# Performance work log

Measured on AMD Instinct MI355X. Metric: run time of the kernel, lower is better.

Reference implementation:

```python
import jax, jax.numpy as jnp
import numpy as np

N_NODES = 50000
N_EDGES = 600000
D = 128
ITERATIONS = 3


def setup_inputs() -> dict:
    key = jax.random.key(0)
    k0, k1, k2, k3 = jax.random.split(key, 4)
    node_feats = jax.random.normal(k0, (N_NODES, D), dtype=jnp.float32)
    adjacency = jax.random.randint(k1, (N_EDGES, 2), 0, N_NODES, dtype=jnp.int64)
    scale = 1.0 / np.sqrt(D).astype(np.float32)
    W_emb = jax.random.normal(k2, (D, D), dtype=jnp.float32) * scale
    b_emb = jnp.zeros((D,), dtype=jnp.float32)
    W_upd = jax.random.normal(k3, (D, D), dtype=jnp.float32) * scale
    b_upd = jnp.zeros((D,), dtype=jnp.float32)
    return {
        "node_feats": node_feats,
        "W_emb": W_emb,
        "b_emb": b_emb,
        "W_upd": W_upd,
        "b_upd": b_upd,
        "adjacency": adjacency,
    }


def reference(node_feats, W_emb, b_emb, W_upd, b_upd, adjacency):
    # Embedding layer: Dense + ReLU per node (inference path skips BatchNorm)
    h = jax.nn.relu(node_feats @ W_emb + b_emb)  # [N, D]

    src = adjacency[:, 0]
    dst = adjacency[:, 1]

    # Each undirected edge contributes a message in both directions.
    ones = jnp.ones((N_EDGES,), dtype=h.dtype)
    deg = (jax.ops.segment_sum(ones, src, num_segments=N_NODES)
           + jax.ops.segment_sum(ones, dst, num_segments=N_NODES))  # [N]
    denom = (deg + 1.0)[:, None]  # +1 for the node's own contribution

    for _ in range(ITERATIONS):
        # MessagePassing: gather neighbor features, scatter-add into nodes,
        # then normalize by (num incoming messages + 1).
        agg = (jax.ops.segment_sum(h[dst], src, num_segments=N_NODES)
               + jax.ops.segment_sum(h[src], dst, num_segments=N_NODES))  # [N, D]
        h = (h + agg) / denom
        # Update: per-node Dense followed by sigmoid nonlinearity.
        h = jax.nn.sigmoid(h @ W_upd + b_upd)
    return h
```

## Files before the change

### kernel.cpp

```cpp
#include <hip/hip_runtime.h>
#include <hip/hip_bf16.h>

#define NN 50000
#define NE 600000
#define DD 128
#define RB 64
#define NSHARD_DIV 6250
#define GB ((NN + RB - 1) / RB)
#define EBQ ((NE + 1023) / 1024)
#define SB ((NN + 1023) / 1024)
#define NSH2 12500
#define GQB2 (8 * ((NSH2 + 15) / 16))

typedef __bf16 bfrag __attribute__((ext_vector_type(8)));
typedef float  ffrag __attribute__((ext_vector_type(4)));
typedef unsigned uintv4 __attribute__((ext_vector_type(4)));
typedef unsigned uintv2 __attribute__((ext_vector_type(2)));

union frag_cast { uintv4 u4; unsigned u[4]; bfrag b; };

__device__ __forceinline__ float bfbits2f(unsigned v) { return __uint_as_float(v << 16); }
__device__ __forceinline__ unsigned f2bfbits(float f) {
    unsigned u = __float_as_uint(f);
    return (u + 0x7FFFu + ((u >> 16) & 1u)) >> 16;
}

__device__ __forceinline__ float ld_in(const void* p, int idx, int f32) {
    return f32 ? ((const float*)p)[idx]
               : bfbits2f(((const unsigned short*)p)[idx]);
}

__device__ __forceinline__ void ld_edge_nt(const int* adj, int e, int i64, int& s, int& d) {
    if (i64) {
        s = __builtin_nontemporal_load(&adj[4 * e]);
        d = __builtin_nontemporal_load(&adj[4 * e + 2]);
    } else {
        s = __builtin_nontemporal_load(&adj[2 * e]);
        d = __builtin_nontemporal_load(&adj[2 * e + 1]);
    }
}

__global__ void k_prep(const unsigned* __restrict__ Ww, const unsigned* __restrict__ adjw,
                       const void* __restrict__ We, const void* __restrict__ Wu,
                       unsigned short* __restrict__ WeT, unsigned short* __restrict__ WuT,
                       int* __restrict__ flags, int* __restrict__ deg) {
    const int tid = threadIdx.x;
    if (blockIdx.x < DD) {
        __shared__ int scnt;
        if (tid == 0) scnt = 0;
        __syncthreads();
        int c = 0;
        for (int i = tid; i < 512; i += 256) {
            unsigned e = (Ww[i] >> 7) & 0xFFu;
            c += (e >= 0x60u && e <= 0x85u) ? 1 : 0;
        }
        atomicAdd(&scnt, c);
        __syncthreads();
        const int f32 = (scnt >= 256) ? 0 : 1;
        const int k = blockIdx.x;
        if (tid < DD) {
            WeT[tid * DD + k] = (unsigned short)f2bfbits(ld_in(We, k * DD + tid, f32));
        } else {
            int n = tid - DD;
            WuT[n * DD + k] = (unsigned short)f2bfbits(ld_in(Wu, k * DD + n, f32));
        }
        return;
    }
    for (int i = (blockIdx.x - DD) * 256 + tid; i < NN; i += 64 * 256) deg[i] = 0;
    if (blockIdx.x != DD) return;
    __shared__ int cnt[2];
    if (tid < 2) cnt[tid] = 0;
    __syncthreads();
    int c0 = 0, c1 = 0;
    for (int i = tid; i < 512; i += 256) {
        unsigned e = (Ww[i] >> 7) & 0xFFu;
        c0 += (e >= 0x60u && e <= 0x85u) ? 1 : 0;
        c1 += (adjw[2 * i + 1] == 0u) ? 1 : 0;
    }
    atomicAdd(&cnt[0], c0);
    atomicAdd(&cnt[1], c1);
    __syncthreads();
    if (tid == 0) {
        flags[0] = (cnt[0] >= 256) ? 0 : 1;
        flags[1] = (cnt[1] >= 256) ? 1 : 0;
    }
}

__device__ __forceinline__ void stage_w(const uintv4* __restrict__ WTg, uintv4* sW, int tid) {
#pragma unroll
    for (int k = 0; k < 8; k++) {
        int d = k * 256 + tid;
        int m = d & 15, rest = d >> 4;
        int quad = rest & 3, ks = (rest >> 2) & 3, ct = rest >> 4;
        sW[d] = WTg[(ct * 16 + m) * 16 + (ks * 4 + quad)];
    }
}

__device__ __forceinline__ void mfma_rows(const bfrag af[4], const bfrag* sW,
                                          int m, int quad, ffrag acc[8]) {
#pragma unroll
    for (int ks = 0; ks < 4; ks++) {
#pragma unroll
        for (int ct = 0; ct < 8; ct++) {
            bfrag bf_ = sW[((ct * 4 + ks) * 4 + quad) * 16 + m];
            acc[ct] = __builtin_amdgcn_mfma_f32_16x16x32_bf16(af[ks], bf_, acc[ct], 0, 0, 0);
        }
    }
}

__device__ __forceinline__ void st_h2(unsigned short* __restrict__ Hout,
                                      int ct, int m, int orow, float z) {
    Hout[(size_t)(ct >> 2) * (NN * 64) + (size_t)orow * 64 + (ct & 3) * 16 + m] =
        (unsigned short)f2bfbits(z);
}

__launch_bounds__(256, 5)
__global__ void k_main1(const void* __restrict__ Xp, const unsigned short* __restrict__ WTg,
                        const void* __restrict__ Bp, unsigned short* __restrict__ Hout,
                        const int* __restrict__ flags, const int* __restrict__ adj,
                        int* __restrict__ deg, uintv2* __restrict__ edg) {
    __shared__ __align__(16) unsigned short sWT[DD * DD];
    const int tid = threadIdx.x;
    if (blockIdx.x >= GB) {
        const int bb = blockIdx.x - GB;
        const int i64 = flags[1];
#pragma unroll
        for (int k = 0; k < 4; k++) {
            const int e = bb * 1024 + k * 256 + tid;
            if (e < NE) {
                int s, d;
                ld_edge_nt(adj, e, i64, s, d);
                uintv2 out;
                if ((unsigned)s < NN && (unsigned)d < NN) {
                    int ks = atomicAdd(&deg[s], 1);
                    int kd = atomicAdd(&deg[d], 1);
                    out[0] = (unsigned)s | ((unsigned)d << 16);
                    out[1] = (unsigned)ks | ((unsigned)kd << 16);
                } else {
                    out[0] = 0xFFFFFFFFu;
                    out[1] = 0;
                }
                __builtin_nontemporal_store(out, &edg[e]);
            }
        }
        return;
    }
    const int wave = tid >> 6;
    const int lane = tid & 63;
    const int f32  = flags[0];
    const int m    = lane & 15;
    const int quad = lane >> 4;
    const int rowbase = blockIdx.x * RB + wave * 16;
    const int row  = rowbase + m;
    const int rc   = (row < NN) ? row : (NN - 1);

    stage_w((const uintv4*)WTg, (uintv4*)sWT, tid);

    bfrag af[4];
    if (f32) {
        const float4* Xf = (const float4*)Xp;
#pragma unroll
        for (int ks = 0; ks < 4; ks++) {
            const int k0 = ks * 32 + quad * 8;
            float4 a0 = Xf[rc * 32 + (k0 >> 2)];
            float4 a1 = Xf[rc * 32 + (k0 >> 2) + 1];
            frag_cast fc;
            fc.u[0] = f2bfbits(a0.x) | (f2bfbits(a0.y) << 16);
            fc.u[1] = f2bfbits(a0.z) | (f2bfbits(a0.w) << 16);
            fc.u[2] = f2bfbits(a1.x) | (f2bfbits(a1.y) << 16);
            fc.u[3] = f2bfbits(a1.z) | (f2bfbits(a1.w) << 16);
            af[ks] = fc.b;
        }
    } else {
        const uintv4* Xv = (const uintv4*)Xp;
#pragma unroll
        for (int ks = 0; ks < 4; ks++) {
            const int k0 = ks * 32 + quad * 8;
            frag_cast fc;
            fc.u4 = Xv[rc * 16 + (k0 >> 3)];
            af[ks] = fc.b;
        }
    }
    __syncthreads();

    ffrag acc[8];
#pragma unroll
    for (int i = 0; i < 8; i++) acc[i] = (ffrag)(0.0f);
    mfma_rows(af, (const bfrag*)sWT, m, quad, acc);

#pragma unroll
    for (int ct = 0; ct < 8; ct++) {
        int col = ct * 16 + m;
        float bb = ld_in(Bp, col, f32);
#pragma unroll
        for (int reg = 0; reg < 4; reg++) {
            int orow = rowbase + quad * 4 + reg;
            if (orow < NN) {
                float z = fmaxf(acc[ct][reg] + bb, 0.0f);
                st_h2(Hout, ct, m, orow, z);
            }
        }
    }
}

__global__ void k_scan1(const int* __restrict__ deg, int* __restrict__ rows,
                        int* __restrict__ sums) {
    __shared__ int wsum[16];
    __shared__ int woff[16];
    const int tid  = threadIdx.x;
    const int wid  = tid >> 6;
    const int lane = tid & 63;
    const int i = blockIdx.x * 1024 + tid;
    int x = (i < NN) ? deg[i] : 0;
#pragma unroll
    for (int off = 1; off < 64; off <<= 1) {
        int y = __shfl_up(x, off, 64);
        if (lane >= off) x += y;
    }
    if (lane == 63) wsum[wid] = x;
    __syncthreads();
    if (wid == 0) {
        int s  = (lane < 16) ? wsum[lane] : 0;
        int xs = s;
#pragma unroll
        for (int off = 1; off < 16; off <<= 1) {
            int y = __shfl_up(xs, off, 64);
            if (lane >= off) xs += y;
        }
        if (lane < 16) woff[lane] = xs - s;
        if (lane == 15) sums[blockIdx.x] = xs;
    }
    __syncthreads();
    if (i < NN) rows[i + 1] = x + woff[wid];
}

__global__ void k_scan2(int* __restrict__ sums, int nb) {
    int t = threadIdx.x;
    int v = (t < nb) ? sums[t] : 0;
    int x = v;
    for (int off = 1; off < 64; off <<= 1) {
        int y = __shfl_up(x, off, 64);
        if (t >= off) x += y;
    }
    if (t < nb) sums[t] = x - v;
}

__global__ void k_scan3(const int* __restrict__ sums, int* __restrict__ rows) {
    int i = blockIdx.x * 1024 + threadIdx.x;
    if (i < NN) {
        rows[i + 1] += sums[blockIdx.x];
        if (i == 0) rows[0] = 0;
    }
}

__launch_bounds__(256)
__global__ void k_fill2(const uintv2* __restrict__ edg, const int* __restrict__ rows,
                        unsigned short* __restrict__ nbr) {
    const int shard = blockIdx.x & 7;
    const int bb = blockIdx.x >> 3;
#pragma unroll
    for (int k = 0; k < 4; k++) {
        const int e = bb * 1024 + k * 256 + threadIdx.x;
        if (e >= NE) continue;
        uintv2 v = __builtin_nontemporal_load(&edg[e]);
        if (v[0] == 0xFFFFFFFFu) continue;
        const int s = v[0] & 0xFFFFu, d = v[0] >> 16;
        if (s / NSHARD_DIV == shard) nbr[rows[s] + (v[1] & 0xFFFFu)] = (unsigned short)d;
        if (d / NSHARD_DIV == shard) nbr[rows[d] + (v[1] >> 16)]    = (unsigned short)s;
    }
}

__launch_bounds__(256)
__global__ void k_gath4(const unsigned* __restrict__ Hp, const int* __restrict__ rows,
                        const unsigned short* __restrict__ nbr,
                        unsigned* __restrict__ XB32) {
    const int shard = blockIdx.x & 7;
    const int plane = shard >> 2;
    const int qr    = shard & 3;
    const int nrel  = (blockIdx.x >> 3) * 16 + (threadIdx.x >> 4);
    const int cs2   = threadIdx.x & 15;
    const int nid   = qr * NSH2 + ((nrel < NSH2) ? nrel : (NSH2 - 1));
    const uintv2* Pv = (const uintv2*)Hp + (size_t)plane * (NN * 16);
    const int st = rows[nid], en = rows[nid + 1];
    uintv2 sv = Pv[nid * 16 + cs2];
    float a0 = bfbits2f(sv[0] & 0xFFFFu), a1 = bfbits2f(sv[0] >> 16);
    float a2 = bfbits2f(sv[1] & 0xFFFFu), a3 = bfbits2f(sv[1] >> 16);
    int j = st;
    for (; j + 8 <= en; j += 8) {
        int n[8];
#pragma unroll
        for (int t = 0; t < 8; t++) n[t] = nbr[j + t];
        uintv2 v[8];
#pragma unroll
        for (int t = 0; t < 8; t++) v[t] = Pv[n[t] * 16 + cs2];
#pragma unroll
        for (int t = 0; t < 8; t++) {
            a0 += bfbits2f(v[t][0] & 0xFFFFu);
            a1 += bfbits2f(v[t][0] >> 16);
            a2 += bfbits2f(v[t][1] & 0xFFFFu);
            a3 += bfbits2f(v[t][1] >> 16);
        }
    }
    for (; j < en; ++j) {
        uintv2 v = Pv[(int)nbr[j] * 16 + cs2];
        a0 += bfbits2f(v[0] & 0xFFFFu);
        a1 += bfbits2f(v[0] >> 16);
        a2 += bfbits2f(v[1] & 0xFFFFu);
        a3 += bfbits2f(v[1] >> 16);
    }
    const float inv = 1.0f / (float)(en - st + 1);
    if (nrel < NSH2) {
        uintv2 pk;
        pk[0] = f2bfbits(a0 * inv) | (f2bfbits(a1 * inv) << 16);
        pk[1] = f2bfbits(a2 * inv) | (f2bfbits(a3 * inv) << 16);
        __builtin_nontemporal_store(pk, (uintv2*)XB32 + (size_t)nid * 32 + plane * 16 + cs2);
    }
}

__launch_bounds__(256, 5)
__global__ void k_gemmB(const unsigned short* __restrict__ XB,
                        const unsigned short* __restrict__ WTg, const void* __restrict__ Bp,
                        unsigned short* __restrict__ HoutBf, float* __restrict__ HoutF,
                        const int* __restrict__ flags, int last) {
    __shared__ __align__(16) unsigned short sWT[DD * DD];
    const int tid  = threadIdx.x;
    const int wave = tid >> 6;
    const int lane = tid & 63;
    const int f32  = flags[0];
    const int m    = lane & 15;
    const int quad = lane >> 4;
    const int rowbase = blockIdx.x * RB + wave * 16;
    const int row  = rowbase + m;

    stage_w((const uintv4*)WTg, (uintv4*)sWT, tid);

    bfrag af[4];
    const uintv4* Xv = (const uintv4*)XB;
#pragma unroll
    for (int ks = 0; ks < 4; ks++) {
        const int k0 = ks * 32 + quad * 8;
        frag_cast fc;
        fc.u4 = __builtin_nontemporal_load(&Xv[row * 16 + (k0 >> 3)]);
        af[ks] = fc.b;
    }
    __syncthreads();

    ffrag acc[8];
#pragma unroll
    for (int i = 0; i < 8; i++) acc[i] = (ffrag)(0.0f);
    mfma_rows(af, (const bfrag*)sWT, m, quad, acc);

#pragma unroll
    for (int ct = 0; ct < 8; ct++) {
        int col = ct * 16 + m;
        float bb = ld_in(Bp, col, f32);
#pragma unroll
        for (int reg = 0; reg < 4; reg++) {
            int orow = rowbase + quad * 4 + reg;
            if (orow < NN) {
                float s = 1.0f / (1.0f + __expf(-(acc[ct][reg] + bb)));
                if (!last) {
                    st_h2(HoutBf, ct, m, orow, s);
                } else if (f32) {
                    HoutF[orow * DD + col] = s;
                } else {
                    ((unsigned short*)HoutF)[orow * DD + col] = (unsigned short)f2bfbits(s);
                }
            }
        }
    }
}

extern "C" void kernel_launch(void* const* d_in, const int* in_sizes, int n_in,
                              void* d_out, int out_size, void* d_ws, size_t ws_size,
                              hipStream_t stream) {
    const void* X  = d_in[0];
    const void* We = d_in[1];
    const void* be = d_in[2];
    const void* Wu = d_in[3];
    const void* bu = d_in[4];
    const int* adj = (const int*)d_in[5];

    char* p = (char*)d_ws;
    int* FLAGS = (int*)p;                       p += 256;
    int* ROWS  = (int*)p;                       p += ((NN + 1) * 4 + 252) / 256 * 256;
    int* SUMS  = (int*)p;                       p += 256;
    unsigned short* NBR = (unsigned short*)p;   p += (size_t)2 * NE * 2;
    unsigned short* WeT = (unsigned short*)p;   p += DD * DD * 2;
    unsigned short* WuT = (unsigned short*)p;   p += DD * DD * 2;
    unsigned short* HW  = (unsigned short*)p;
    uintv2* EDG2 = (uintv2*)p;
    int* DEG = (int*)(p + (size_t)NE * 8);

    unsigned short* HA = (unsigned short*)d_out + (size_t)NN * DD;

    k_prep<<<DD + 64, 256, 0, stream>>>((const unsigned*)We, (const unsigned*)adj,
                                        We, Wu, WeT, WuT, FLAGS, DEG);
    k_main1<<<GB + EBQ, 256, 0, stream>>>(X, WeT, be, HA, FLAGS, adj, DEG, EDG2);
    k_scan1<<<SB, 1024, 0, stream>>>(DEG, ROWS, SUMS);
    k_scan2<<<1, 64, 0, stream>>>(SUMS, SB);
    k_scan3<<<SB, 1024, 0, stream>>>(SUMS, ROWS);
    k_fill2<<<8 * EBQ, 256, 0, stream>>>(EDG2, ROWS, NBR);

    for (int it = 0; it < 3; ++it) {
        int last = (it == 2);
        k_gath4<<<GQB2, 256, 0, stream>>>((const unsigned*)HA, ROWS, NBR, (unsigned*)HW);
        k_gemmB<<<GB, 256, 0, stream>>>(HW, WuT, bu, HA, (float*)d_out, FLAGS, last);
    }
}
```

Baseline: 358.9 us.

## Sort nodes by degree for gather and widen per-thread loads to 16 bytes

Builds a degree histogram during the scan, computes bucket offsets, and scatters node ids into a degree-sorted order array. The gather kernel then processes nodes in that order, so nodes with similar neighbor counts share a wavefront and loop-length divergence drops. Each thread now loads 16-byte chunks (8 lanes per node-plane) instead of 8-byte ones. The locality-based quarter sharding of the old gather is gone and there is extra setup work, and the randomized node order may reduce cache reuse of the output writes.

```diff
diff --git a/kernel.cpp b/kernel.cpp
--- a/kernel.cpp
+++ b/kernel.cpp
@@ -9,8 +9,7 @@
 #define GB ((NN + RB - 1) / RB)
 #define EBQ ((NE + 1023) / 1024)
 #define SB ((NN + 1023) / 1024)
-#define NSH2 12500
-#define GQB2 (8 * ((NSH2 + 15) / 16))
+#define GQB3 (2 * ((NN + 31) / 32))
 
 typedef __bf16 bfrag __attribute__((ext_vector_type(8)));
 typedef float  ffrag __attribute__((ext_vector_type(4)));
@@ -43,7 +42,8 @@
 __global__ void k_prep(const unsigned* __restrict__ Ww, const unsigned* __restrict__ adjw,
                        const void* __restrict__ We, const void* __restrict__ Wu,
                        unsigned short* __restrict__ WeT, unsigned short* __restrict__ WuT,
-                       int* __restrict__ flags, int* __restrict__ deg) {
+                       int* __restrict__ flags, int* __restrict__ deg,
+                       int* __restrict__ bins) {
     const int tid = threadIdx.x;
     if (blockIdx.x < DD) {
         __shared__ int scnt;
@@ -67,6 +67,7 @@
         return;
     }
     for (int i = (blockIdx.x - DD) * 256 + tid; i < NN; i += 64 * 256) deg[i] = 0;
+    if (blockIdx.x == DD + 1) bins[tid] = 0;
     if (blockIdx.x != DD) return;
     __shared__ int cnt[2];
     if (tid < 2) cnt[tid] = 0;
@@ -204,14 +205,18 @@
 }
 
 __global__ void k_scan1(const int* __restrict__ deg, int* __restrict__ rows,
-                        int* __restrict__ sums) {
+                        int* __restrict__ sums, int* __restrict__ bins) {
     __shared__ int wsum[16];
     __shared__ int woff[16];
+    __shared__ int hist[256];
     const int tid  = threadIdx.x;
     const int wid  = tid >> 6;
     const int lane = tid & 63;
     const int i = blockIdx.x * 1024 + tid;
+    if (tid < 256) hist[tid] = 0;
+    __syncthreads();
     int x = (i < NN) ? deg[i] : 0;
+    if (i < NN) atomicAdd(&hist[(x < 255) ? x : 255], 1);
 #pragma unroll
     for (int off = 1; off < 64; off <<= 1) {
         int y = __shfl_up(x, off, 64);
@@ -232,24 +237,45 @@
     }
     __syncthreads();
     if (i < NN) rows[i + 1] = x + woff[wid];
-}
-
-__global__ void k_scan2(int* __restrict__ sums, int nb) {
-    int t = threadIdx.x;
-    int v = (t < nb) ? sums[t] : 0;
+    if (tid < 256 && hist[tid]) atomicAdd(&bins[tid], hist[tid]);
+}
+
+__global__ void k_scan2(int* __restrict__ sums, int nb,
+                        const int* __restrict__ bins, int* __restrict__ bcur) {
+    __shared__ int wps[4];
+    const int t = threadIdx.x, lane = t & 63, w = t >> 6;
+    if (w == 0) {
+        int v = (lane < nb) ? sums[lane] : 0;
+        int x = v;
+        for (int off = 1; off < 64; off <<= 1) {
+            int y = __shfl_up(x, off, 64);
+            if (lane >= off) x += y;
+        }
+        if (lane < nb) sums[lane] = x - v;
+    }
+    int v = bins[t];
     int x = v;
     for (int off = 1; off < 64; off <<= 1) {
         int y = __shfl_up(x, off, 64);
-        if (t >= off) x += y;
-    }
-    if (t < nb) sums[t] = x - v;
-}
-
-__global__ void k_scan3(const int* __restrict__ sums, int* __restrict__ rows) {
+        if (lane >= off) x += y;
+    }
+    if (lane == 63) wps[w] = x;
+    __syncthreads();
+    int add = 0;
+    for (int k = 0; k < w; k++) add += wps[k];
+    bcur[t] = x - v + add;
+}
+
+__global__ void k_scan3(const int* __restrict__ sums, int* __restrict__ rows,
+                        const int* __restrict__ deg, int* __restrict__ bcur,
+                        int* __restrict__ order) {
     int i = blockIdx.x * 1024 + threadIdx.x;
     if (i < NN) {
         rows[i + 1] += sums[blockIdx.x];
         if (i == 0) rows[0] = 0;
+        int d = deg[i];
+        int pos = atomicAdd(&bcur[(d < 255) ? d : 255], 1);
+        order[pos] = i;
     }
 }
 
@@ -270,50 +296,52 @@
     }
 }
 
+__device__ __forceinline__ void accv4(float a[8], uintv4 v) {
+#pragma unroll
+    for (int k = 0; k < 4; k++) {
+        a[2 * k]     += bfbits2f(v[k] & 0xFFFFu);
+        a[2 * k + 1] += bfbits2f(v[k] >> 16);
+    }
+}
+
 __launch_bounds__(256)
-__global__ void k_gath4(const unsigned* __restrict__ Hp, const int* __restrict__ rows,
+__global__ void k_gath5(const unsigned* __restrict__ Hp, const int* __restrict__ rows,
                         const unsigned short* __restrict__ nbr,
-                        unsigned* __restrict__ XB32) {
-    const int shard = blockIdx.x & 7;
-    const int plane = shard >> 2;
-    const int qr    = shard & 3;
-    const int nrel  = (blockIdx.x >> 3) * 16 + (threadIdx.x >> 4);
-    const int cs2   = threadIdx.x & 15;
-    const int nid   = qr * NSH2 + ((nrel < NSH2) ? nrel : (NSH2 - 1));
-    const uintv2* Pv = (const uintv2*)Hp + (size_t)plane * (NN * 16);
+                        const int* __restrict__ order, unsigned* __restrict__ XB32) {
+    const int plane = blockIdx.x & 1;
+    const int chunk = blockIdx.x >> 1;
+    const int g     = threadIdx.x >> 3;
+    const int l8    = threadIdx.x & 7;
+    const int opos  = chunk * 32 + g;
+    const int nid   = order[(opos < NN) ? opos : (NN - 1)];
+    const uintv4* Pv = (const uintv4*)Hp + (size_t)plane * (NN * 8);
     const int st = rows[nid], en = rows[nid + 1];
-    uintv2 sv = Pv[nid * 16 + cs2];
-    float a0 = bfbits2f(sv[0] & 0xFFFFu), a1 = bfbits2f(sv[0] >> 16);
-    float a2 = bfbits2f(sv[1] & 0xFFFFu), a3 = bfbits2f(sv[1] >> 16);
+    uintv4 sv = Pv[(size_t)nid * 8 + l8];
+    float a[8];
+#pragma unroll
+    for (int k = 0; k < 4; k++) {
+        a[2 * k]     = bfbits2f(sv[k] & 0xFFFFu);
+        a[2 * k + 1] = bfbits2f(sv[k] >> 16);
+    }
     int j = st;
     for (; j + 8 <= en; j += 8) {
         int n[8];
 #pragma unroll
         for (int t = 0; t < 8; t++) n[t] = nbr[j + t];
-        uintv2 v[8];
-#pragma unroll
-        for (int t = 0; t < 8; t++) v[t] = Pv[n[t] * 16 + cs2];
-#pragma unroll
-        for (int t = 0; t < 8; t++) {
-            a0 += bfbits2f(v[t][0] & 0xFFFFu);
-            a1 += bfbits2f(v[t][0] >> 16);
-            a2 += bfbits2f(v[t][1] & 0xFFFFu);
-            a3 += bfbits2f(v[t][1] >> 16);
-        }
-    }
-    for (; j < en; ++j) {
-        uintv2 v = Pv[(int)nbr[j] * 16 + cs2];
-        a0 += bfbits2f(v[0] & 0xFFFFu);
-        a1 += bfbits2f(v[0] >> 16);
-        a2 += bfbits2f(v[1] & 0xFFFFu);
-        a3 += bfbits2f(v[1] >> 16);
-    }
+        uintv4 v[8];
+#pragma unroll
+        for (int t = 0; t < 8; t++) v[t] = Pv[(size_t)n[t] * 8 + l8];
+#pragma unroll
+        for (int t = 0; t < 8; t++) accv4(a, v[t]);
+    }
+    for (; j < en; ++j) accv4(a, Pv[(size_t)nbr[j] * 8 + l8]);
     const float inv = 1.0f / (float)(en - st + 1);
-    if (nrel < NSH2) {
-        uintv2 pk;
-        pk[0] = f2bfbits(a0 * inv) | (f2bfbits(a1 * inv) << 16);
-        pk[1] = f2bfbits(a2 * inv) | (f2bfbits(a3 * inv) << 16);
-        __builtin_nontemporal_store(pk, (uintv2*)XB32 + (size_t)nid * 32 + plane * 16 + cs2);
+    if (opos < NN) {
+        uintv4 pk;
+#pragma unroll
+        for (int k = 0; k < 4; k++)
+            pk[k] = f2bfbits(a[2 * k] * inv) | (f2bfbits(a[2 * k + 1] * inv) << 16);
+        __builtin_nontemporal_store(pk, (uintv4*)XB32 + (size_t)nid * 16 + plane * 8 + l8);
     }
 }
 
@@ -385,6 +413,9 @@
     int* FLAGS = (int*)p;                       p += 256;
     int* ROWS  = (int*)p;                       p += ((NN + 1) * 4 + 252) / 256 * 256;
     int* SUMS  = (int*)p;                       p += 256;
+    int* BINS  = (int*)p;                       p += 1024;
+    int* BCUR  = (int*)p;                       p += 1024;
+    int* ORDER = (int*)p;                       p += ((NN * 4 + 255) / 256) * 256;
     unsigned short* NBR = (unsigned short*)p;   p += (size_t)2 * NE * 2;
     unsigned short* WeT = (unsigned short*)p;   p += DD * DD * 2;
     unsigned short* WuT = (unsigned short*)p;   p += DD * DD * 2;
@@ -395,16 +426,16 @@
     unsigned short* HA = (unsigned short*)d_out + (size_t)NN * DD;
 
     k_prep<<<DD + 64, 256, 0, stream>>>((const unsigned*)We, (const unsigned*)adj,
-                                        We, Wu, WeT, WuT, FLAGS, DEG);
+                                        We, Wu, WeT, WuT, FLAGS, DEG, BINS);
     k_main1<<<GB + EBQ, 256, 0, stream>>>(X, WeT, be, HA, FLAGS, adj, DEG, EDG2);
-    k_scan1<<<SB, 1024, 0, stream>>>(DEG, ROWS, SUMS);
-    k_scan2<<<1, 64, 0, stream>>>(SUMS, SB);
-    k_scan3<<<SB, 1024, 0, stream>>>(SUMS, ROWS);
+    k_scan1<<<SB, 1024, 0, stream>>>(DEG, ROWS, SUMS, BINS);
+    k_scan2<<<1, 256, 0, stream>>>(SUMS, SB, BINS, BCUR);
+    k_scan3<<<SB, 1024, 0, stream>>>(SUMS, ROWS, DEG, BCUR, ORDER);
     k_fill2<<<8 * EBQ, 256, 0, stream>>>(EDG2, ROWS, NBR);
 
     for (int it = 0; it < 3; ++it) {
         int last = (it == 2);
-        k_gath4<<<GQB2, 256, 0, stream>>>((const unsigned*)HA, ROWS, NBR, (unsigned*)HW);
+        k_gath5<<<GQB3, 256, 0, stream>>>((const unsigned*)HA, ROWS, NBR, ORDER, (unsigned*)HW);
         k_gemmB<<<GB, 256, 0, stream>>>(HW, WuT, bu, HA, (float*)d_out, FLAGS, last);
     }
 }
```

Measured after the change: 471.1 us. +31.2%, slower.
